# Kernel tuning notes

Measured on AMD Instinct MI355X. Metric: run time of the kernel, lower is better.

Reference implementation:

```python
import jax, jax.numpy as jnp
import numpy as np

BS, NWP, D, NEXP, H, OUT = 32768, 10, 256, 6, 64, 2

def setup_inputs() -> dict:
    key = jax.random.key(0)
    ks = jax.random.split(key, 8)
    x = jax.random.normal(ks[0], (BS, NWP, D), dtype=jnp.float32)
    measurements = jax.random.randint(ks[1], (BS, 1), 0, NEXP, dtype=jnp.int32)
    rank_embed = 0.02 * jax.random.normal(ks[2], (1, NWP, D), dtype=jnp.float32)
    # Linear weights stored as [in, out] for einsum; biases [out]
    W1 = 0.05 * jax.random.normal(ks[3], (NEXP, D, H), dtype=jnp.float32)
    b1 = 0.05 * jax.random.normal(ks[4], (NEXP, H), dtype=jnp.float32)
    W2 = 0.05 * jax.random.normal(ks[5], (NEXP, H, OUT), dtype=jnp.float32)
    b2 = 0.05 * jax.random.normal(ks[6], (NEXP, OUT), dtype=jnp.float32)
    return {"x": x, "measurements": measurements, "rank_embed": rank_embed,
            "W1": W1, "b1": b1, "W2": W2, "b2": b2}

def reference(x, measurements, rank_embed, W1, b1, W2, b2):
    command = measurements[:, 0]                      # [bs] int in [0,6)
    xr = x + rank_embed                               # [bs, 10, d]
    # Dense 6-way expert MLP (matches original: all heads computed for all samples)
    h = jax.nn.relu(jnp.einsum('bnd,edh->benh', xr, W1) + b1[None, :, None, :])  # [bs,6,10,64]
    wp = jnp.einsum('benh,eho->beno', h, W2) + b2[None, :, None, :]              # [bs,6,10,2]
    sel = jnp.take_along_axis(wp, command[:, None, None, None].astype(jnp.int32), axis=1)[:, 0]  # [bs,10,2]
    return jnp.cumsum(sel, axis=1)
```

## Files before the change

kernel.cpp:

```cpp
#include <hip/hip_runtime.h>
#include <hip/hip_bf16.h>

#define BS 32768
#define NWP 10
#define DD 256
#define NEXP 6
#define HH 64
#define OUT_DIM 2
#define MB 32
#define MAXQ 1032

typedef short bf16x8 __attribute__((ext_vector_type(8)));
typedef float f32x4 __attribute__((ext_vector_type(4)));

__device__ inline short bfs(float f) {
  __hip_bfloat16 h = __float2bfloat16(f);
  return __builtin_bit_cast(short, h);
}

__global__ __launch_bounds__(1024) void bucket_k(const int* __restrict__ cmd,
                                                 int* __restrict__ counts,
                                                 int* __restrict__ lists) {
  __shared__ int wcnt[16][NEXP];
  __shared__ int wbase[16][NEXP];
  const int tid = threadIdx.x;
  const int w = tid >> 6, lane = tid & 63;
  const int b = blockIdx.x * 1024 + tid;
  const int e = cmd[b];
  #pragma unroll
  for (int ee = 0; ee < NEXP; ++ee) {
    unsigned long long m = __ballot(e == ee);
    if (lane == 0) wcnt[w][ee] = __popcll(m);
  }
  __syncthreads();
  if (tid < NEXP) {
    int tot = 0, pf[16];
    #pragma unroll
    for (int ww = 0; ww < 16; ++ww) { pf[ww] = tot; tot += wcnt[ww][tid]; }
    const int bb = atomicAdd(&counts[tid], tot);
    #pragma unroll
    for (int ww = 0; ww < 16; ++ww) wbase[ww][tid] = bb + pf[ww];
  }
  __syncthreads();
  #pragma unroll
  for (int ee = 0; ee < NEXP; ++ee) {
    unsigned long long m = __ballot(e == ee);
    if (e == ee) {
      const int nbelow = __popcll(m & ((1ull << lane) - 1ull));
      lists[ee * BS + wbase[w][ee] + nbelow] = b;
    }
  }
}

__global__ void prep_k(const float* __restrict__ W1,
                       const float* __restrict__ re,
                       const float* __restrict__ b1,
                       short* __restrict__ W1T,
                       float* __restrict__ rw) {
  const int e = blockIdx.x;
  const int part = blockIdx.y;
  if (part < 8) {
    const int h = part * 8 + (threadIdx.x >> 5);
    const int d0 = (threadIdx.x & 31) * 8;
    const float* wp = W1 + (size_t)e * DD * HH + h;
    bf16x8 v;
    #pragma unroll
    for (int i = 0; i < 8; ++i) v[i] = bfs(wp[(size_t)(d0 + i) * HH]);
    *(bf16x8*)(W1T + ((size_t)e * HH + h) * DD + d0) = v;
  } else {
    for (int i = threadIdx.x; i < NWP * HH; i += 256) {
      const int n = i >> 6, h = i & 63;
      const float* rp = re + (size_t)n * DD;
      const float* wp = W1 + (size_t)e * DD * HH + h;
      float s = b1[e * HH + h];
      for (int d = 0; d < DD; ++d) s += rp[d] * wp[(size_t)d * HH];
      rw[((size_t)e * NWP + n) * HH + h] = s;
    }
  }
}

__global__ void build_q_k(const int* __restrict__ counts, int* __restrict__ qmeta) {
  __shared__ int base[NEXP + 1];
  if (threadIdx.x == 0) {
    int tot = 0;
    #pragma unroll
    for (int e = 0; e < NEXP; ++e) {
      base[e] = tot;
      tot += (counts[e] + MB - 1) / MB;
    }
    base[NEXP] = tot;
    qmeta[17] = tot;
  }
  __syncthreads();
  #pragma unroll
  for (int e = 0; e < NEXP; ++e) {
    const int ne = base[e + 1] - base[e];
    for (int j = threadIdx.x; j < ne; j += blockDim.x)
      qmeta[32 + base[e] + j] = (e << 16) | (j * MB);
  }
}

__global__ __launch_bounds__(256, 2) void moe_gemm_k(
    const float* __restrict__ x,
    const short* __restrict__ W1T,
    const float* __restrict__ rwg,
    const float* __restrict__ W2,
    const float* __restrict__ b2,
    const int* __restrict__ qmeta,
    const int* __restrict__ lists,
    float* __restrict__ out)
{
  __shared__ short Xa[4][16 * DD];
  __shared__ float rwl[NWP][68];
  __shared__ float w2l[HH * OUT_DIM];
  __shared__ float po[MB * NWP][2];

  const int wi = blockIdx.x;
  if (wi >= qmeta[17]) return;
  const int ent = qmeta[32 + wi];
  const int e = ent >> 16;
  const int start = ent & 0xffff;
  const int cnt = qmeta[e];
  const int nb = min(MB, cnt - start);
  const int nrows = nb * NWP;

  const int tid = threadIdx.x;
  const int lane = tid & 63;
  const int wv = tid >> 6;
  const int arow = lane & 15;
  const int ag = lane >> 4;

  bf16x8 Wf[4][8];
  {
    const short* wb = W1T + ((size_t)e * HH + arow) * DD + ag * 8;
    #pragma unroll
    for (int nt = 0; nt < 4; ++nt)
      #pragma unroll
      for (int ks = 0; ks < 8; ++ks)
        Wf[nt][ks] = *(const bf16x8*)(wb + (size_t)(nt * 16) * DD + ks * 32);
  }
  for (int i = tid; i < NWP * HH; i += 256)
    rwl[i >> 6][i & 63] = rwg[(size_t)e * NWP * HH + i];
  if (tid < HH * OUT_DIM) w2l[tid] = W2[(size_t)e * HH * OUT_DIM + tid];

  __syncthreads();

  short* Xw = &Xa[wv][0];
  const int ntile = (nrows + 15) >> 4;
  const int lbase = e * BS + start;

  for (int t = wv; t < ntile; t += 4) {
    #pragma unroll
    for (int r = 0; r < 16; ++r) {
      const int rowu = __builtin_amdgcn_readfirstlane(min(t * 16 + r, nrows - 1));
      const int item = rowu / NWP;
      const int nn = rowu - item * NWP;
      const int gb = lists[lbase + item];
      const float4 xv = *(const float4*)(x + ((size_t)gb * NWP + nn) * DD + lane * 4);
      short4 pk = make_short4(bfs(xv.x), bfs(xv.y), bfs(xv.z), bfs(xv.w));
      *(short4*)&Xw[r * DD + ((lane * 4) ^ ((r & 7) << 3))] = pk;
    }

    f32x4 acc[4] = {{0,0,0,0},{0,0,0,0},{0,0,0,0},{0,0,0,0}};
    #pragma unroll
    for (int ks = 0; ks < 8; ++ks) {
      const int kidx = ks * 32 + ag * 8;
      const bf16x8 bx = *(const bf16x8*)&Xw[arow * DD + (kidx ^ ((arow & 7) << 3))];
      #pragma unroll
      for (int nt = 0; nt < 4; ++nt)
        acc[nt] = __builtin_amdgcn_mfma_f32_16x16x32_bf16(Wf[nt][ks], bx, acc[nt], 0, 0, 0);
    }

    const int row = t * 16 + arow;
    const int rowc = min(row, nrows - 1);
    const int nn = rowc - (rowc / NWP) * NWP;
    float p0 = 0.f, p1 = 0.f;
    #pragma unroll
    for (int nt = 0; nt < 4; ++nt) {
      const int h0 = nt * 16 + ag * 4;
      const float4 rv = *(const float4*)&rwl[nn][h0];
      const float4 wa = *(const float4*)&w2l[h0 * 2];
      const float4 wb = *(const float4*)&w2l[h0 * 2 + 4];
      const float h0v = fmaxf(acc[nt][0] + rv.x, 0.f);
      const float h1v = fmaxf(acc[nt][1] + rv.y, 0.f);
      const float h2v = fmaxf(acc[nt][2] + rv.z, 0.f);
      const float h3v = fmaxf(acc[nt][3] + rv.w, 0.f);
      p0 += h0v * wa.x + h1v * wa.z + h2v * wb.x + h3v * wb.z;
      p1 += h0v * wa.y + h1v * wa.w + h2v * wb.y + h3v * wb.w;
    }
    p0 += __shfl_xor(p0, 16); p1 += __shfl_xor(p1, 16);
    p0 += __shfl_xor(p0, 32); p1 += __shfl_xor(p1, 32);
    if (ag == 0 && row < nrows) {
      po[row][0] = p0;
      po[row][1] = p1;
    }
  }

  __syncthreads();

  if (tid < nb) {
    const int gb = lists[lbase + tid];
    const float bb0 = b2[e * OUT_DIM + 0];
    const float bb1 = b2[e * OUT_DIM + 1];
    float v[NWP * OUT_DIM];
    float s0 = 0.f, s1 = 0.f;
    #pragma unroll
    for (int n = 0; n < NWP; ++n) {
      s0 += po[tid * NWP + n][0] + bb0;
      s1 += po[tid * NWP + n][1] + bb1;
      v[n * 2 + 0] = s0;
      v[n * 2 + 1] = s1;
    }
    float4* op = (float4*)(out + (size_t)gb * NWP * OUT_DIM);
    #pragma unroll
    for (int q = 0; q < 5; ++q)
      op[q] = make_float4(v[q * 4], v[q * 4 + 1], v[q * 4 + 2], v[q * 4 + 3]);
  }
}

extern "C" void kernel_launch(void* const* d_in, const int* in_sizes, int n_in,
                              void* d_out, int out_size, void* d_ws, size_t ws_size,
                              hipStream_t stream) {
  const float* x          = (const float*)d_in[0];
  const int*   meas       = (const int*)d_in[1];
  const float* rank_embed = (const float*)d_in[2];
  const float* W1         = (const float*)d_in[3];
  const float* b1         = (const float*)d_in[4];
  const float* W2         = (const float*)d_in[5];
  const float* b2         = (const float*)d_in[6];
  float* out = (float*)d_out;

  int* qmeta = (int*)d_ws;
  int* lists = (int*)((char*)d_ws + 8192);
  short* W1T = (short*)((char*)d_ws + (800 << 10));
  float* rw  = (float*)((char*)d_ws + (1000 << 10));

  hipMemsetAsync(d_ws, 0, 8192, stream);
  bucket_k<<<BS / 1024, 1024, 0, stream>>>(meas, qmeta, lists);
  prep_k<<<dim3(NEXP, 9), 256, 0, stream>>>(W1, rank_embed, b1, W1T, rw);
  build_q_k<<<1, 256, 0, stream>>>(qmeta, qmeta);
  moe_gemm_k<<<MAXQ, 256, 0, stream>>>(x, W1T, rw, W2, b2, qmeta, lists, out);
}
```

Measured before the change: 111.6 us.

## Double-buffer x tiles via async global_load_lds and drop queue-build kernel

Replaces synchronous per-row x loads and bf16 conversion into shared memory with async global-to-LDS fp32 loads into a double buffer, so the next tile's loads overlap the current tile's MFMA work, and converts to bf16 after reading from LDS. Each block now derives its expert and start offset directly from the counts, which removes the build_q_k launch. Batch indices are cached in LDS, and blocks shrink to 128 threads with one block per CU in the launch bounds. The trade-off is fewer waves per block and more LDS traffic, since tiles are stored in fp32.

```diff
diff --git a/kernel.cpp b/kernel.cpp
--- a/kernel.cpp
+++ b/kernel.cpp
@@ -12,6 +12,8 @@
 
 typedef short bf16x8 __attribute__((ext_vector_type(8)));
 typedef float f32x4 __attribute__((ext_vector_type(4)));
+typedef __attribute__((address_space(3))) void as3void;
+typedef const __attribute__((address_space(1))) void as1void;
 
 __device__ inline short bfs(float f) {
   __hip_bfloat16 h = __float2bfloat16(f);
@@ -79,28 +81,11 @@
   }
 }
 
-__global__ void build_q_k(const int* __restrict__ counts, int* __restrict__ qmeta) {
-  __shared__ int base[NEXP + 1];
-  if (threadIdx.x == 0) {
-    int tot = 0;
-    #pragma unroll
-    for (int e = 0; e < NEXP; ++e) {
-      base[e] = tot;
-      tot += (counts[e] + MB - 1) / MB;
-    }
-    base[NEXP] = tot;
-    qmeta[17] = tot;
-  }
-  __syncthreads();
-  #pragma unroll
-  for (int e = 0; e < NEXP; ++e) {
-    const int ne = base[e + 1] - base[e];
-    for (int j = threadIdx.x; j < ne; j += blockDim.x)
-      qmeta[32 + base[e] + j] = (e << 16) | (j * MB);
-  }
-}
-
-__global__ __launch_bounds__(256, 2) void moe_gemm_k(
+#define DSR(I, OFF) \
+  asm volatile("ds_read_b128 %0, %1 offset:" OFF : "=v"(ra[I]) : "v"(a0)); \
+  asm volatile("ds_read_b128 %0, %1 offset:" OFF : "=v"(rb[I]) : "v"(a1));
+
+__global__ __launch_bounds__(128, 1) void moe_gemm_k(
     const float* __restrict__ x,
     const short* __restrict__ W1T,
     const float* __restrict__ rwg,
@@ -110,16 +95,21 @@
     const int* __restrict__ lists,
     float* __restrict__ out)
 {
-  __shared__ short Xa[4][16 * DD];
+  __shared__ float Xa[2][2][16 * DD];
   __shared__ float rwl[NWP][68];
   __shared__ float w2l[HH * OUT_DIM];
   __shared__ float po[MB * NWP][2];
+  __shared__ int bidl[MB];
 
   const int wi = blockIdx.x;
-  if (wi >= qmeta[17]) return;
-  const int ent = qmeta[32 + wi];
-  const int e = ent >> 16;
-  const int start = ent & 0xffff;
+  int acc0 = 0, e = -1, start = 0;
+  #pragma unroll
+  for (int ee = 0; ee < NEXP; ++ee) {
+    const int nc = (qmeta[ee] + MB - 1) >> 5;
+    if (e < 0 && wi < acc0 + nc) { e = ee; start = (wi - acc0) * MB; }
+    acc0 += nc;
+  }
+  if (e < 0) return;
   const int cnt = qmeta[e];
   const int nb = min(MB, cnt - start);
   const int nrows = nb * NWP;
@@ -129,6 +119,7 @@
   const int wv = tid >> 6;
   const int arow = lane & 15;
   const int ag = lane >> 4;
+  const int lbase = e * BS + start;
 
   bf16x8 Wf[4][8];
   {
@@ -139,33 +130,58 @@
       for (int ks = 0; ks < 8; ++ks)
         Wf[nt][ks] = *(const bf16x8*)(wb + (size_t)(nt * 16) * DD + ks * 32);
   }
-  for (int i = tid; i < NWP * HH; i += 256)
+  for (int i = tid; i < NWP * HH; i += 128)
     rwl[i >> 6][i & 63] = rwg[(size_t)e * NWP * HH + i];
   if (tid < HH * OUT_DIM) w2l[tid] = W2[(size_t)e * HH * OUT_DIM + tid];
-
-  __syncthreads();
-
-  short* Xw = &Xa[wv][0];
+  if (tid < nb) bidl[tid] = lists[lbase + tid];
+
+  asm volatile("s_waitcnt vmcnt(0)" ::: "memory");
+  __syncthreads();
+
   const int ntile = (nrows + 15) >> 4;
-  const int lbase = e * BS + start;
-
-  for (int t = wv; t < ntile; t += 4) {
+
+  const unsigned wb0 =
+      (unsigned)(uintptr_t)(as3void*)&Xa[wv][0][0];
+  const unsigned pk = (unsigned)((arow & 7) << 4);
+  const unsigned roff = (unsigned)(arow * 1024) + (((unsigned)(ag * 32)) ^ pk);
+
+  auto issue = [&](int t, int b) {
     #pragma unroll
     for (int r = 0; r < 16; ++r) {
-      const int rowu = __builtin_amdgcn_readfirstlane(min(t * 16 + r, nrows - 1));
+      const int rowu = min(t * 16 + r, nrows - 1);
       const int item = rowu / NWP;
       const int nn = rowu - item * NWP;
-      const int gb = lists[lbase + item];
-      const float4 xv = *(const float4*)(x + ((size_t)gb * NWP + nn) * DD + lane * 4);
-      short4 pk = make_short4(bfs(xv.x), bfs(xv.y), bfs(xv.z), bfs(xv.w));
-      *(short4*)&Xw[r * DD + ((lane * 4) ^ ((r & 7) << 3))] = pk;
-    }
+      const int gb = bidl[item];
+      const float* src = x + ((size_t)gb * NWP + nn) * DD
+                       + ((((unsigned)lane * 16) ^ ((unsigned)(r & 7) << 4)) >> 2);
+      __builtin_amdgcn_global_load_lds((as1void*)src,
+                                       (as3void*)&Xa[wv][b][r * DD], 16, 0, 0);
+    }
+  };
+
+  issue(wv, 0);
+  int cur = 0;
+  for (int t = wv; t < ntile; t += 2) {
+    issue(t + 2, cur ^ 1);
+    asm volatile("s_waitcnt vmcnt(16)" ::: "memory");
+    __builtin_amdgcn_sched_barrier(0);
+
+    const unsigned a0 = wb0 + (cur ? 16384u : 0u) + roff;
+    const unsigned a1 = a0 ^ 16u;
+    f32x4 ra[8], rb[8];
+    DSR(0, "0")   DSR(1, "128") DSR(2, "256") DSR(3, "384")
+    DSR(4, "512") DSR(5, "640") DSR(6, "768") DSR(7, "896")
+    asm volatile("s_waitcnt lgkmcnt(0)" ::: "memory");
+    __builtin_amdgcn_sched_barrier(0);
 
     f32x4 acc[4] = {{0,0,0,0},{0,0,0,0},{0,0,0,0},{0,0,0,0}};
     #pragma unroll
     for (int ks = 0; ks < 8; ++ks) {
-      const int kidx = ks * 32 + ag * 8;
-      const bf16x8 bx = *(const bf16x8*)&Xw[arow * DD + (kidx ^ ((arow & 7) << 3))];
+      bf16x8 bx;
+      bx[0] = bfs(ra[ks][0]); bx[1] = bfs(ra[ks][1]);
+      bx[2] = bfs(ra[ks][2]); bx[3] = bfs(ra[ks][3]);
+      bx[4] = bfs(rb[ks][0]); bx[5] = bfs(rb[ks][1]);
+      bx[6] = bfs(rb[ks][2]); bx[7] = bfs(rb[ks][3]);
       #pragma unroll
       for (int nt = 0; nt < 4; ++nt)
         acc[nt] = __builtin_amdgcn_mfma_f32_16x16x32_bf16(Wf[nt][ks], bx, acc[nt], 0, 0, 0);
@@ -194,12 +210,13 @@
       po[row][0] = p0;
       po[row][1] = p1;
     }
+    cur ^= 1;
   }
 
   __syncthreads();
 
   if (tid < nb) {
-    const int gb = lists[lbase + tid];
+    const int gb = bidl[tid];
     const float bb0 = b2[e * OUT_DIM + 0];
     const float bb1 = b2[e * OUT_DIM + 1];
     float v[NWP * OUT_DIM];
@@ -238,6 +255,5 @@
   hipMemsetAsync(d_ws, 0, 8192, stream);
   bucket_k<<<BS / 1024, 1024, 0, stream>>>(meas, qmeta, lists);
   prep_k<<<dim3(NEXP, 9), 256, 0, stream>>>(W1, rank_embed, b1, W1T, rw);
-  build_q_k<<<1, 256, 0, stream>>>(qmeta, qmeta);
-  moe_gemm_k<<<MAXQ, 256, 0, stream>>>(x, W1T, rw, W2, b2, qmeta, lists, out);
-}
+  moe_gemm_k<<<MAXQ, 128, 0, stream>>>(x, W1T, rw, W2, b2, qmeta, lists, out);
+}
```

Result: faster. 108.1 us (-3.2%).

## Merge bucketing and weight prep into one kernel, drop queue-build kernel

Applied to the files above, without the earlier changes.

Combines the bucketing, weight transpose/convert and rank-embed precompute kernels into a single 50-block launch. Removes the queue-build kernel by having each GEMM block derive its expert and start offset from the per-expert counts. The memset shrinks, and x loads become nontemporal to avoid polluting cache. This cuts launch count and serialization between small kernels, at the cost of a short per-block prefix loop and larger blocks for the prep work.

```diff
diff --git a/kernel.cpp b/kernel.cpp
--- a/kernel.cpp
+++ b/kernel.cpp
@@ -18,85 +18,65 @@
   return __builtin_bit_cast(short, h);
 }
 
-__global__ __launch_bounds__(1024) void bucket_k(const int* __restrict__ cmd,
-                                                 int* __restrict__ counts,
-                                                 int* __restrict__ lists) {
-  __shared__ int wcnt[16][NEXP];
-  __shared__ int wbase[16][NEXP];
+__global__ __launch_bounds__(1024) void aux_k(const int* __restrict__ cmd,
+                                              const float* __restrict__ W1,
+                                              const float* __restrict__ re,
+                                              const float* __restrict__ b1,
+                                              int* __restrict__ counts,
+                                              int* __restrict__ lists,
+                                              short* __restrict__ W1T,
+                                              float* __restrict__ rw) {
+  const int bid = blockIdx.x;
   const int tid = threadIdx.x;
-  const int w = tid >> 6, lane = tid & 63;
-  const int b = blockIdx.x * 1024 + tid;
-  const int e = cmd[b];
-  #pragma unroll
-  for (int ee = 0; ee < NEXP; ++ee) {
-    unsigned long long m = __ballot(e == ee);
-    if (lane == 0) wcnt[w][ee] = __popcll(m);
-  }
-  __syncthreads();
-  if (tid < NEXP) {
-    int tot = 0, pf[16];
-    #pragma unroll
-    for (int ww = 0; ww < 16; ++ww) { pf[ww] = tot; tot += wcnt[ww][tid]; }
-    const int bb = atomicAdd(&counts[tid], tot);
-    #pragma unroll
-    for (int ww = 0; ww < 16; ++ww) wbase[ww][tid] = bb + pf[ww];
-  }
-  __syncthreads();
-  #pragma unroll
-  for (int ee = 0; ee < NEXP; ++ee) {
-    unsigned long long m = __ballot(e == ee);
-    if (e == ee) {
-      const int nbelow = __popcll(m & ((1ull << lane) - 1ull));
-      lists[ee * BS + wbase[w][ee] + nbelow] = b;
-    }
-  }
-}
-
-__global__ void prep_k(const float* __restrict__ W1,
-                       const float* __restrict__ re,
-                       const float* __restrict__ b1,
-                       short* __restrict__ W1T,
-                       float* __restrict__ rw) {
-  const int e = blockIdx.x;
-  const int part = blockIdx.y;
-  if (part < 8) {
-    const int h = part * 8 + (threadIdx.x >> 5);
-    const int d0 = (threadIdx.x & 31) * 8;
+
+  if (bid < 32) {
+    __shared__ int wcnt[16][NEXP];
+    __shared__ int wbase[16][NEXP];
+    const int w = tid >> 6, lane = tid & 63;
+    const int b = bid * 1024 + tid;
+    const int e = cmd[b];
+    #pragma unroll
+    for (int ee = 0; ee < NEXP; ++ee) {
+      unsigned long long m = __ballot(e == ee);
+      if (lane == 0) wcnt[w][ee] = __popcll(m);
+    }
+    __syncthreads();
+    if (tid < NEXP) {
+      int tot = 0, pf[16];
+      #pragma unroll
+      for (int ww = 0; ww < 16; ++ww) { pf[ww] = tot; tot += wcnt[ww][tid]; }
+      const int bb = atomicAdd(&counts[tid], tot);
+      #pragma unroll
+      for (int ww = 0; ww < 16; ++ww) wbase[ww][tid] = bb + pf[ww];
+    }
+    __syncthreads();
+    #pragma unroll
+    for (int ee = 0; ee < NEXP; ++ee) {
+      unsigned long long m = __ballot(e == ee);
+      if (e == ee) {
+        const int nbelow = __popcll(m & ((1ull << lane) - 1ull));
+        lists[ee * BS + wbase[w][ee] + nbelow] = b;
+      }
+    }
+  } else if (bid < 44) {
+    const int e = (bid - 32) >> 1;
+    const int h = ((bid - 32) & 1) * 32 + (tid >> 5);
+    const int d0 = (tid & 31) * 8;
     const float* wp = W1 + (size_t)e * DD * HH + h;
     bf16x8 v;
     #pragma unroll
     for (int i = 0; i < 8; ++i) v[i] = bfs(wp[(size_t)(d0 + i) * HH]);
     *(bf16x8*)(W1T + ((size_t)e * HH + h) * DD + d0) = v;
   } else {
-    for (int i = threadIdx.x; i < NWP * HH; i += 256) {
-      const int n = i >> 6, h = i & 63;
+    const int e = bid - 44;
+    if (tid < NWP * HH) {
+      const int n = tid >> 6, h = tid & 63;
       const float* rp = re + (size_t)n * DD;
       const float* wp = W1 + (size_t)e * DD * HH + h;
       float s = b1[e * HH + h];
       for (int d = 0; d < DD; ++d) s += rp[d] * wp[(size_t)d * HH];
       rw[((size_t)e * NWP + n) * HH + h] = s;
     }
-  }
-}
-
-__global__ void build_q_k(const int* __restrict__ counts, int* __restrict__ qmeta) {
-  __shared__ int base[NEXP + 1];
-  if (threadIdx.x == 0) {
-    int tot = 0;
-    #pragma unroll
-    for (int e = 0; e < NEXP; ++e) {
-      base[e] = tot;
-      tot += (counts[e] + MB - 1) / MB;
-    }
-    base[NEXP] = tot;
-    qmeta[17] = tot;
-  }
-  __syncthreads();
-  #pragma unroll
-  for (int e = 0; e < NEXP; ++e) {
-    const int ne = base[e + 1] - base[e];
-    for (int j = threadIdx.x; j < ne; j += blockDim.x)
-      qmeta[32 + base[e] + j] = (e << 16) | (j * MB);
   }
 }
 
@@ -116,10 +96,14 @@
   __shared__ float po[MB * NWP][2];
 
   const int wi = blockIdx.x;
-  if (wi >= qmeta[17]) return;
-  const int ent = qmeta[32 + wi];
-  const int e = ent >> 16;
-  const int start = ent & 0xffff;
+  int acc0 = 0, e = -1, start = 0;
+  #pragma unroll
+  for (int ee = 0; ee < NEXP; ++ee) {
+    const int nc = (qmeta[ee] + MB - 1) >> 5;
+    if (e < 0 && wi < acc0 + nc) { e = ee; start = (wi - acc0) * MB; }
+    acc0 += nc;
+  }
+  if (e < 0) return;
   const int cnt = qmeta[e];
   const int nb = min(MB, cnt - start);
   const int nrows = nb * NWP;
@@ -129,6 +113,7 @@
   const int wv = tid >> 6;
   const int arow = lane & 15;
   const int ag = lane >> 4;
+  const int lbase = e * BS + start;
 
   bf16x8 Wf[4][8];
   {
@@ -147,7 +132,6 @@
 
   short* Xw = &Xa[wv][0];
   const int ntile = (nrows + 15) >> 4;
-  const int lbase = e * BS + start;
 
   for (int t = wv; t < ntile; t += 4) {
     #pragma unroll
@@ -156,8 +140,9 @@
       const int item = rowu / NWP;
       const int nn = rowu - item * NWP;
       const int gb = lists[lbase + item];
-      const float4 xv = *(const float4*)(x + ((size_t)gb * NWP + nn) * DD + lane * 4);
-      short4 pk = make_short4(bfs(xv.x), bfs(xv.y), bfs(xv.z), bfs(xv.w));
+      const f32x4 xv = __builtin_nontemporal_load(
+          (const f32x4*)(x + ((size_t)gb * NWP + nn) * DD + lane * 4));
+      short4 pk = make_short4(bfs(xv[0]), bfs(xv[1]), bfs(xv[2]), bfs(xv[3]));
       *(short4*)&Xw[r * DD + ((lane * 4) ^ ((r & 7) << 3))] = pk;
     }
 
@@ -235,9 +220,7 @@
   short* W1T = (short*)((char*)d_ws + (800 << 10));
   float* rw  = (float*)((char*)d_ws + (1000 << 10));
 
-  hipMemsetAsync(d_ws, 0, 8192, stream);
-  bucket_k<<<BS / 1024, 1024, 0, stream>>>(meas, qmeta, lists);
-  prep_k<<<dim3(NEXP, 9), 256, 0, stream>>>(W1, rank_embed, b1, W1T, rw);
-  build_q_k<<<1, 256, 0, stream>>>(qmeta, qmeta);
+  hipMemsetAsync(d_ws, 0, 256, stream);
+  aux_k<<<50, 1024, 0, stream>>>(meas, W1, rank_embed, b1, qmeta, lists, W1T, rw);
   moe_gemm_k<<<MAXQ, 256, 0, stream>>>(x, W1T, rw, W2, b2, qmeta, lists, out);
 }
```

New measurement: 101.1 us (median of 2 runs). 1.1x faster.
